# Kernel tuning notes

Hardware: AMD Instinct MI355X
Metric: run time of the kernel (lower is better)

## Reference

```python
import jax, jax.numpy as jnp
import numpy as np

MIN_ROUGHNESS = 0.08
MAX_ROUGHNESS = 0.5
N_MIPS = 6  # 512 -> 16 cubemap mip chain


def _safe_normalize(x, eps=1e-20):
    return x * jax.lax.rsqrt(jnp.clip(jnp.sum(x * x, -1, keepdims=True), eps, None))


def _dot(a, b):
    return jnp.sum(a * b, -1, keepdims=True)


def _cube_face_uv(d):
    # nvdiffrast cube addressing (matches util.cube_to_dir face layout)
    x, y, z = d[..., 0], d[..., 1], d[..., 2]
    ax, ay, az = jnp.abs(x), jnp.abs(y), jnp.abs(z)
    is_x = (ax >= ay) & (ax >= az)
    is_y = (~is_x) & (ay >= az)
    face = jnp.where(is_x, jnp.where(x >= 0, 0, 1),
           jnp.where(is_y, jnp.where(y >= 0, 2, 3), jnp.where(z >= 0, 4, 5)))
    ma = jnp.maximum(jnp.where(is_x, ax, jnp.where(is_y, ay, az)), 1e-20)
    u = jnp.where(face == 0, -z, jnp.where(face == 1, z, jnp.where(face == 5, -x, x))) / ma
    v = jnp.where(face == 2, z, jnp.where(face == 3, -z, -y)) / ma
    return face, u, v


def _bilinear_cube(tex, face, u, v):
    # tex: [6,R,R,C]; face/u/v: [...]; edge-clamped bilinear within the face
    R = tex.shape[1]
    tu = (u * 0.5 + 0.5) * R - 0.5
    tv = (v * 0.5 + 0.5) * R - 0.5
    x0 = jnp.floor(tu); y0 = jnp.floor(tv)
    fx = (tu - x0)[..., None]; fy = (tv - y0)[..., None]
    x0i = jnp.clip(x0, 0, R - 1).astype(jnp.int32)
    x1i = jnp.clip(x0 + 1, 0, R - 1).astype(jnp.int32)
    y0i = jnp.clip(y0, 0, R - 1).astype(jnp.int32)
    y1i = jnp.clip(y0 + 1, 0, R - 1).astype(jnp.int32)
    c00 = tex[face, y0i, x0i]; c01 = tex[face, y0i, x1i]
    c10 = tex[face, y1i, x0i]; c11 = tex[face, y1i, x1i]
    return (c00 * (1 - fx) + c01 * fx) * (1 - fy) + (c10 * (1 - fx) + c11 * fx) * fy


def _sample_cubemap(tex, dirs):
    f, u, v = _cube_face_uv(dirs)
    return _bilinear_cube(tex, f, u, v)


def _sample_2d_clamp(tex, uv):
    # tex: [H,W,C]; uv in [0,1]^2, clamp boundary bilinear (FG LUT lookup)
    H, W = tex.shape[0], tex.shape[1]
    tu = uv[..., 0] * W - 0.5
    tv = uv[..., 1] * H - 0.5
    x0 = jnp.floor(tu); y0 = jnp.floor(tv)
    fx = (tu - x0)[..., None]; fy = (tv - y0)[..., None]
    x0i = jnp.clip(x0, 0, W - 1).astype(jnp.int32)
    x1i = jnp.clip(x0 + 1, 0, W - 1).astype(jnp.int32)
    y0i = jnp.clip(y0, 0, H - 1).astype(jnp.int32)
    y1i = jnp.clip(y0 + 1, 0, H - 1).astype(jnp.int32)
    c00 = tex[y0i, x0i]; c01 = tex[y0i, x1i]
    c10 = tex[y1i, x0i]; c11 = tex[y1i, x1i]
    return (c00 * (1 - fx) + c01 * fx) * (1 - fy) + (c10 * (1 - fx) + c11 * fx) * fy


def _get_mip(r, n_levels):
    lo = (jnp.clip(r, MIN_ROUGHNESS, MAX_ROUGHNESS) - MIN_ROUGHNESS) / (MAX_ROUGHNESS - MIN_ROUGHNESS) * (n_levels - 2)
    hi = (jnp.clip(r, MAX_ROUGHNESS, 1.0) - MAX_ROUGHNESS) / (1.0 - MAX_ROUGHNESS) + (n_levels - 2)
    return jnp.where(r < MAX_ROUGHNESS, lo, hi)


def _linear2srgb(x):
    xs = jnp.where(x > 0.0031308, x, 1.0)  # avoid pow(0) grad issues
    return jnp.where(x > 0.0031308, 1.055 * jnp.power(xs, 1.0 / 2.4) - 0.055, 12.92 * x)


def _avg_pool_cube(c):
    F, R, _, C = c.shape
    return c.reshape(F, R // 2, 2, R // 2, 2, C).mean(axis=(2, 4))


def setup_inputs() -> dict:
    key = jax.random.key(0)
    ks = jax.random.split(key, 10)
    B, H, W = 1, 1024, 1024
    gb_pos = jax.random.normal(ks[0], (B, H, W, 3), jnp.float32)
    gb_normal = _safe_normalize(jax.random.normal(ks[1], (B, H, W, 3), jnp.float32))
    basecolor = jax.random.uniform(ks[2], (B, H, W, 3), jnp.float32)
    metallic = jax.random.uniform(ks[3], (B, H, W, 1), jnp.float32)
    roughness = jax.random.uniform(ks[4], (B, H, W, 1), jnp.float32)
    view_pos = jax.random.normal(ks[5], (1, 1, 1, 3), jnp.float32) * 3.0
    diffuse = jax.random.uniform(ks[6], (6, 16, 16, 3), jnp.float32)
    fg_lut = jax.random.uniform(ks[7], (256, 256, 2), jnp.float32)
    specs = {}
    s = jax.random.uniform(ks[8], (6, 512, 512, 3), jnp.float32)
    for l in range(N_MIPS):
        specs['spec%d' % l] = s
        if l < N_MIPS - 1:
            s = _avg_pool_cube(s)
    return dict(gb_pos=gb_pos, gb_normal=gb_normal, basecolor=basecolor,
                metallic=metallic, roughness=roughness, view_pos=view_pos,
                diffuse=diffuse, fg_lut=fg_lut, **specs)


def reference(gb_pos, gb_normal, basecolor, metallic, roughness, view_pos,
              diffuse, fg_lut, spec0, spec1, spec2, spec3, spec4, spec5):
    specs = [spec0, spec1, spec2, spec3, spec4, spec5]
    L = len(specs)
    metallic = metallic[..., :1]
    wo = _safe_normalize(view_pos - gb_pos)
    diffuse_albedo = (1.0 - metallic) * basecolor
    specular_albedo = 0.04 * (1.0 - metallic) + metallic * basecolor
    reflvec = _safe_normalize(2.0 * _dot(wo, gb_normal) * gb_normal - wo)
    # diffuse IBL: cubemap gather along normal
    ambient = _sample_cubemap(diffuse, gb_normal)
    diffuse_linear = ambient * diffuse_albedo
    # FG LUT gather
    NdotV = jnp.clip(_dot(wo, gb_normal), 1e-4, None)
    fg = _sample_2d_clamp(fg_lut, jnp.concatenate([NdotV, roughness], -1))
    # trilinear (linear-mipmap-linear) specular cubemap gather
    mip = jnp.clip(_get_mip(roughness[..., 0], L), 0.0, L - 1.0)
    face, u, v = _cube_face_uv(reflvec)
    spec = jnp.zeros(gb_pos.shape[:-1] + (spec0.shape[-1],), gb_pos.dtype)
    for l in range(L):
        w = jnp.clip(1.0 - jnp.abs(mip - l), 0.0, 1.0)[..., None]
        spec = spec + w * _bilinear_cube(specs[l], face, u, v)
    reflectance = specular_albedo * fg[..., 0:1] + fg[..., 1:2]
    rgb = spec * reflectance + diffuse_linear
    return _linear2srgb(jnp.clip(rgb, 0.0, 1.0))
```

## Files before the change

kernel.cpp:

```cpp
#include <hip/hip_runtime.h>

struct V3 { float x, y, z; };

__device__ __forceinline__ V3 v3add(V3 a, V3 b){ return {a.x+b.x, a.y+b.y, a.z+b.z}; }
__device__ __forceinline__ V3 v3sub(V3 a, V3 b){ return {a.x-b.x, a.y-b.y, a.z-b.z}; }
__device__ __forceinline__ V3 v3scale(V3 a, float s){ return {a.x*s, a.y*s, a.z*s}; }
__device__ __forceinline__ V3 v3mul(V3 a, V3 b){ return {a.x*b.x, a.y*b.y, a.z*b.z}; }
__device__ __forceinline__ float dot3(V3 a, V3 b){ return fmaf(a.x,b.x, fmaf(a.y,b.y, a.z*b.z)); }
__device__ __forceinline__ V3 nrm3(V3 a){
    float s = rsqrtf(fmaxf(dot3(a,a), 1e-20f));
    return v3scale(a, s);
}

#define OFF0 0
#define OFF1 1572864
#define OFF2 1966080
#define OFF3 2064384
#define OFF4 2088960
#define OFF5 2095104
#define DIFF_OFF 2096640
#define TOTAL_TEXELS 2098176
#define WS_BYTES_NEEDED (TOTAL_TEXELS * 16)

__device__ __forceinline__ void cube_face_uv(V3 d, int& face, float& u, float& v){
    float ax = fabsf(d.x), ay = fabsf(d.y), az = fabsf(d.z);
    bool is_x = (ax >= ay) && (ax >= az);
    bool is_y = (!is_x) && (ay >= az);
    face = is_x ? (d.x >= 0.f ? 0 : 1)
                : (is_y ? (d.y >= 0.f ? 2 : 3)
                        : (d.z >= 0.f ? 4 : 5));
    float ma = fmaxf(is_x ? ax : (is_y ? ay : az), 1e-20f);
    float un = (face == 0) ? -d.z : (face == 1) ? d.z : (face == 5) ? -d.x : d.x;
    float vn = (face == 2) ?  d.z : (face == 3) ? -d.z : -d.y;
    float inv = 1.0f / ma;
    u = un * inv;
    v = vn * inv;
}

struct BilinCoord { int x0i, x1i, y0i, y1i; float fx, fy; };

__device__ __forceinline__ BilinCoord bilin_coord(float u, float v, int R){
    float Rf = (float)R;
    float tu = fmaf(fmaf(u, 0.5f, 0.5f), Rf, -0.5f);
    float tv = fmaf(fmaf(v, 0.5f, 0.5f), Rf, -0.5f);
    float x0 = floorf(tu), y0 = floorf(tv);
    BilinCoord c;
    c.fx = tu - x0; c.fy = tv - y0;
    c.x0i = min(max((int)x0,     0), R-1);
    c.x1i = min(max((int)x0 + 1, 0), R-1);
    c.y0i = min(max((int)y0,     0), R-1);
    c.y1i = min(max((int)y0 + 1, 0), R-1);
    return c;
}

__device__ __forceinline__ V3 bilinear_cube4(const float4* __restrict__ tex, int R,
                                             int face, float u, float v){
    BilinCoord c = bilin_coord(u, v, R);
    const float4* base = tex + (size_t)face * R * R;
    const float4* r0 = base + (size_t)c.y0i * R;
    const float4* r1 = base + (size_t)c.y1i * R;
    float4 a = r0[c.x0i];
    float4 b = r0[c.x1i];
    float4 d = r1[c.x0i];
    float4 e = r1[c.x1i];
    float w00 = (1.f-c.fx)*(1.f-c.fy), w01 = c.fx*(1.f-c.fy);
    float w10 = (1.f-c.fx)*c.fy,       w11 = c.fx*c.fy;
    V3 out;
    out.x = a.x*w00 + b.x*w01 + d.x*w10 + e.x*w11;
    out.y = a.y*w00 + b.y*w01 + d.y*w10 + e.y*w11;
    out.z = a.z*w00 + b.z*w01 + d.z*w10 + e.z*w11;
    return out;
}

__device__ __forceinline__ V3 bilinear_cube3(const float* __restrict__ tex, int R,
                                             int face, float u, float v){
    BilinCoord c = bilin_coord(u, v, R);
    const float* base = tex + (size_t)face * R * R * 3;
    const float* r0 = base + (size_t)c.y0i * R * 3;
    const float* r1 = base + (size_t)c.y1i * R * 3;
    const float* p00 = r0 + 3*c.x0i;
    const float* p01 = r0 + 3*c.x1i;
    const float* p10 = r1 + 3*c.x0i;
    const float* p11 = r1 + 3*c.x1i;
    float a0 = p00[0], a1 = p00[1], a2 = p00[2];
    float b0 = p01[0], b1 = p01[1], b2 = p01[2];
    float d0 = p10[0], d1 = p10[1], d2 = p10[2];
    float e0 = p11[0], e1 = p11[1], e2 = p11[2];
    float w00 = (1.f-c.fx)*(1.f-c.fy), w01 = c.fx*(1.f-c.fy);
    float w10 = (1.f-c.fx)*c.fy,       w11 = c.fx*c.fy;
    V3 out;
    out.x = a0*w00 + b0*w01 + d0*w10 + e0*w11;
    out.y = a1*w00 + b1*w01 + d1*w10 + e1*w11;
    out.z = a2*w00 + b2*w01 + d2*w10 + e2*w11;
    return out;
}

__device__ __forceinline__ void sample_fg(const float* __restrict__ lut,
                                          float u, float v, float& fa, float& fb){
    const int W = 256, H = 256;
    float tu = fmaf(u, (float)W, -0.5f);
    float tv = fmaf(v, (float)H, -0.5f);
    float x0 = floorf(tu), y0 = floorf(tv);
    float fx = tu - x0,    fy = tv - y0;
    int x0i = min(max((int)x0,     0), W-1);
    int x1i = min(max((int)x0 + 1, 0), W-1);
    int y0i = min(max((int)y0,     0), H-1);
    int y1i = min(max((int)y0 + 1, 0), H-1);
    const float2* l2 = (const float2*)lut;
    float2 a = l2[(size_t)y0i*W + x0i];
    float2 b = l2[(size_t)y0i*W + x1i];
    float2 d = l2[(size_t)y1i*W + x0i];
    float2 e = l2[(size_t)y1i*W + x1i];
    float w00 = (1.f-fx)*(1.f-fy), w01 = fx*(1.f-fy);
    float w10 = (1.f-fx)*fy,       w11 = fx*fy;
    fa = a.x*w00 + b.x*w01 + d.x*w10 + e.x*w11;
    fb = a.y*w00 + b.y*w01 + d.y*w10 + e.y*w11;
}

__device__ __forceinline__ float lin2srgb(float x){
    float xs = (x > 0.0031308f) ? x : 1.0f;
    float p  = __builtin_amdgcn_exp2f(__builtin_amdgcn_logf(xs) * (1.0f/2.4f));
    return (x > 0.0031308f) ? fmaf(1.055f, p, -0.055f) : 12.92f * x;
}

__device__ __forceinline__ float clamp01(float x){ return fminf(fmaxf(x, 0.f), 1.f); }

__global__ __launch_bounds__(256)
void pack_kernel(const float* __restrict__ s0, const float* __restrict__ s1,
                 const float* __restrict__ s2, const float* __restrict__ s3,
                 const float* __restrict__ s4, const float* __restrict__ s5,
                 const float* __restrict__ diffuse,
                 float4* __restrict__ ws)
{
    int t = blockIdx.x * blockDim.x + threadIdx.x;
    if (t >= TOTAL_TEXELS) return;
    const float* src; int local;
    if      (t >= DIFF_OFF) { src = diffuse; local = t - DIFF_OFF; }
    else if (t >= OFF5)     { src = s5;      local = t - OFF5; }
    else if (t >= OFF4)     { src = s4;      local = t - OFF4; }
    else if (t >= OFF3)     { src = s3;      local = t - OFF3; }
    else if (t >= OFF2)     { src = s2;      local = t - OFF2; }
    else if (t >= OFF1)     { src = s1;      local = t - OFF1; }
    else                    { src = s0;      local = t; }
    float a = src[3*local], b = src[3*local+1], c = src[3*local+2];
    ws[t] = make_float4(a, b, c, 0.f);
}

template <bool PACKED>
__device__ __forceinline__ void shade_pixel(
    int i,
    const float* __restrict__ gb_pos, const float* __restrict__ gb_normal,
    const float* __restrict__ basecolor, const float* __restrict__ metallic,
    const float* __restrict__ roughness, const float* __restrict__ view_pos,
    const float* __restrict__ diffuse, const float* __restrict__ fg_lut,
    const float* __restrict__ s0, const float* __restrict__ s1,
    const float* __restrict__ s2, const float* __restrict__ s3,
    const float* __restrict__ s4, const float* __restrict__ s5,
    const float4* __restrict__ ws,
    float* __restrict__ out)
{
    V3 pos = { gb_pos[3*i],    gb_pos[3*i+1],    gb_pos[3*i+2] };
    V3 nrm = { gb_normal[3*i], gb_normal[3*i+1], gb_normal[3*i+2] };
    V3 bc  = { basecolor[3*i], basecolor[3*i+1], basecolor[3*i+2] };
    float m = metallic[i];
    float r = roughness[i];
    V3 vp  = { view_pos[0], view_pos[1], view_pos[2] };

    V3 wo = nrm3(v3sub(vp, pos));
    float ndv_raw = dot3(wo, nrm);
    V3 refl = nrm3(v3sub(v3scale(nrm, 2.0f*ndv_raw), wo));

    float one_m = 1.0f - m;
    V3 diff_alb = v3scale(bc, one_m);
    V3 spec_alb = { fmaf(m, bc.x, 0.04f*one_m),
                    fmaf(m, bc.y, 0.04f*one_m),
                    fmaf(m, bc.z, 0.04f*one_m) };

    const float MIN_R = 0.08f, MAX_R = 0.5f;
    float lo = (fminf(fmaxf(r, MIN_R), MAX_R) - MIN_R) / (MAX_R - MIN_R) * 4.0f;
    float hi = (fminf(fmaxf(r, MAX_R), 1.0f) - MAX_R) / (1.0f - MAX_R) + 4.0f;
    float mip = (r < MAX_R) ? lo : hi;
    mip = fminf(fmaxf(mip, 0.0f), 5.0f);
    int l0 = min((int)mip, 5);
    float f = mip - (float)l0;
    int l1 = min(l0 + 1, 5);

    int dface; float du, dv;
    cube_face_uv(nrm, dface, du, dv);
    int sface; float su, sv;
    cube_face_uv(refl, sface, su, sv);
    float NdotV = fmaxf(ndv_raw, 0.0001f);

    V3 ambient, specA, specB;
    if (PACKED) {
        int offA = OFF0;
        offA = (l0 == 1) ? OFF1 : offA; offA = (l0 == 2) ? OFF2 : offA;
        offA = (l0 == 3) ? OFF3 : offA; offA = (l0 == 4) ? OFF4 : offA;
        offA = (l0 == 5) ? OFF5 : offA;
        int offB = OFF0;
        offB = (l1 == 1) ? OFF1 : offB; offB = (l1 == 2) ? OFF2 : offB;
        offB = (l1 == 3) ? OFF3 : offB; offB = (l1 == 4) ? OFF4 : offB;
        offB = (l1 == 5) ? OFF5 : offB;
        ambient = bilinear_cube4(ws + DIFF_OFF, 16, dface, du, dv);
        specA   = bilinear_cube4(ws + offA, 512 >> l0, sface, su, sv);
        specB   = bilinear_cube4(ws + offB, 512 >> l1, sface, su, sv);
    } else {
        const float* tA = s0;
        tA = (l0 == 1) ? s1 : tA; tA = (l0 == 2) ? s2 : tA;
        tA = (l0 == 3) ? s3 : tA; tA = (l0 == 4) ? s4 : tA; tA = (l0 == 5) ? s5 : tA;
        const float* tB = s0;
        tB = (l1 == 1) ? s1 : tB; tB = (l1 == 2) ? s2 : tB;
        tB = (l1 == 3) ? s3 : tB; tB = (l1 == 4) ? s4 : tB; tB = (l1 == 5) ? s5 : tB;
        ambient = bilinear_cube3(diffuse, 16, dface, du, dv);
        specA   = bilinear_cube3(tA, 512 >> l0, sface, su, sv);
        specB   = bilinear_cube3(tB, 512 >> l1, sface, su, sv);
    }

    float fa, fb;
    sample_fg(fg_lut, NdotV, r, fa, fb);

    V3 spec = { specA.x + (specB.x - specA.x) * f,
                specA.y + (specB.y - specA.y) * f,
                specA.z + (specB.z - specA.z) * f };
    V3 reflc = { fmaf(spec_alb.x, fa, fb),
                 fmaf(spec_alb.y, fa, fb),
                 fmaf(spec_alb.z, fa, fb) };
    V3 rgb = v3add(v3mul(spec, reflc), v3mul(ambient, diff_alb));

    out[3*i+0] = lin2srgb(clamp01(rgb.x));
    out[3*i+1] = lin2srgb(clamp01(rgb.y));
    out[3*i+2] = lin2srgb(clamp01(rgb.z));
}

template <bool PACKED>
__global__ __launch_bounds__(256)
void envlight_kernel(const float* __restrict__ gb_pos,
                     const float* __restrict__ gb_normal,
                     const float* __restrict__ basecolor,
                     const float* __restrict__ metallic,
                     const float* __restrict__ roughness,
                     const float* __restrict__ view_pos,
                     const float* __restrict__ diffuse,
                     const float* __restrict__ fg_lut,
                     const float* __restrict__ s0,
                     const float* __restrict__ s1,
                     const float* __restrict__ s2,
                     const float* __restrict__ s3,
                     const float* __restrict__ s4,
                     const float* __restrict__ s5,
                     const float4* __restrict__ ws,
                     float* __restrict__ out,
                     int n)
{
    int i = blockIdx.x * blockDim.x + threadIdx.x;
    if (i >= n) return;
    shade_pixel<PACKED>(i, gb_pos, gb_normal, basecolor, metallic, roughness,
                        view_pos, diffuse, fg_lut, s0, s1, s2, s3, s4, s5, ws, out);
}

extern "C" void kernel_launch(void* const* d_in, const int* in_sizes, int n_in,
                              void* d_out, int out_size, void* d_ws, size_t ws_size,
                              hipStream_t stream) {
    const float* gb_pos    = (const float*)d_in[0];
    const float* gb_normal = (const float*)d_in[1];
    const float* basecolor = (const float*)d_in[2];
    const float* metallic  = (const float*)d_in[3];
    const float* roughness = (const float*)d_in[4];
    const float* view_pos  = (const float*)d_in[5];
    const float* diffuse   = (const float*)d_in[6];
    const float* fg_lut    = (const float*)d_in[7];
    const float* s0        = (const float*)d_in[8];
    const float* s1        = (const float*)d_in[9];
    const float* s2        = (const float*)d_in[10];
    const float* s3        = (const float*)d_in[11];
    const float* s4        = (const float*)d_in[12];
    const float* s5        = (const float*)d_in[13];
    float* out = (float*)d_out;

    int n = in_sizes[0] / 3;
    int block = 256;
    int grid = (n + block - 1) / block;

    if (ws_size >= (size_t)WS_BYTES_NEEDED) {
        float4* ws = (float4*)d_ws;
        int pgrid = (TOTAL_TEXELS + block - 1) / block;
        pack_kernel<<<pgrid, block, 0, stream>>>(s0, s1, s2, s3, s4, s5, diffuse, ws);
        envlight_kernel<true><<<grid, block, 0, stream>>>(gb_pos, gb_normal, basecolor,
            metallic, roughness, view_pos, diffuse, fg_lut,
            s0, s1, s2, s3, s4, s5, ws, out, n);
    } else {
        envlight_kernel<false><<<grid, block, 0, stream>>>(gb_pos, gb_normal, basecolor,
            metallic, roughness, view_pos, diffuse, fg_lut,
            s0, s1, s2, s3, s4, s5, (const float4*)nullptr, out, n);
    }
}
```

Before: 184.2 us.

## Pack horizontal texel pairs as fp16 blocks to halve gathers per bilinear tap

The pack kernel now stores each texel together with its right neighbour as six fp16 values in a 16-byte block, instead of one fp32 RGB texel padded to a float4. Each bilinear lookup then needs two 16-byte loads, one per row, rather than four. The left edge is handled by zeroing fx when x0 is negative, and the right edge by duplicating the last texel in each row. This cuts the number of scattered gather transactions, but texture values lose precision to fp16 and the pack kernel does double reads.

```diff
diff --git a/kernel.cpp b/kernel.cpp
--- a/kernel.cpp
+++ b/kernel.cpp
@@ -1,4 +1,5 @@
 #include <hip/hip_runtime.h>
+#include <hip/hip_fp16.h>
 
 struct V3 { float x, y, z; };
 
@@ -12,6 +13,8 @@
     return v3scale(a, s);
 }
 
+struct __align__(16) PairBlock { __half2 h01, h23, h45, h67; };
+
 #define OFF0 0
 #define OFF1 1572864
 #define OFF2 1966080
@@ -19,8 +22,8 @@
 #define OFF4 2088960
 #define OFF5 2095104
 #define DIFF_OFF 2096640
-#define TOTAL_TEXELS 2098176
-#define WS_BYTES_NEEDED (TOTAL_TEXELS * 16)
+#define TOTAL_BLOCKS 2098176
+#define WS_BYTES_NEEDED (TOTAL_BLOCKS * 16)
 
 __device__ __forceinline__ void cube_face_uv(V3 d, int& face, float& u, float& v){
     float ax = fabsf(d.x), ay = fabsf(d.y), az = fabsf(d.z);
@@ -37,57 +40,54 @@
     v = vn * inv;
 }
 
-struct BilinCoord { int x0i, x1i, y0i, y1i; float fx, fy; };
-
-__device__ __forceinline__ BilinCoord bilin_coord(float u, float v, int R){
+__device__ __forceinline__ void pair_extract(const PairBlock& pb, V3& lo, V3& hi){
+    lo.x = __low2float(pb.h01);  lo.y = __high2float(pb.h01); lo.z = __low2float(pb.h23);
+    hi.x = __high2float(pb.h23); hi.y = __low2float(pb.h45);  hi.z = __high2float(pb.h45);
+}
+
+__device__ __forceinline__ V3 bilinear_pairtex(const PairBlock* __restrict__ lvl, int R,
+                                               int face, float u, float v){
+    float Rf = (float)R;
+    float tu = fmaf(fmaf(u, 0.5f, 0.5f), Rf, -0.5f);
+    float tv = fmaf(fmaf(v, 0.5f, 0.5f), Rf, -0.5f);
+    float x0f = floorf(tu), y0f = floorf(tv);
+    float fx = tu - x0f,    fy = tv - y0f;
+    int x0 = (int)x0f;
+    fx = (x0 < 0) ? 0.f : fx;
+    int xb  = min(max(x0, 0), R-1);
+    int y0i = min(max((int)y0f,     0), R-1);
+    int y1i = min(max((int)y0f + 1, 0), R-1);
+    const PairBlock* fb = lvl + (size_t)face * R * R;
+    PairBlock b0 = fb[(size_t)y0i * R + xb];
+    PairBlock b1 = fb[(size_t)y1i * R + xb];
+    V3 l0, h0, l1, h1;
+    pair_extract(b0, l0, h0);
+    pair_extract(b1, l1, h1);
+    V3 r0 = { l0.x + (h0.x-l0.x)*fx, l0.y + (h0.y-l0.y)*fx, l0.z + (h0.z-l0.z)*fx };
+    V3 r1 = { l1.x + (h1.x-l1.x)*fx, l1.y + (h1.y-l1.y)*fx, l1.z + (h1.z-l1.z)*fx };
+    return { r0.x + (r1.x-r0.x)*fy, r0.y + (r1.y-r0.y)*fy, r0.z + (r1.z-r0.z)*fy };
+}
+
+__device__ __forceinline__ V3 bilinear_cube3(const float* __restrict__ tex, int R,
+                                             int face, float u, float v){
     float Rf = (float)R;
     float tu = fmaf(fmaf(u, 0.5f, 0.5f), Rf, -0.5f);
     float tv = fmaf(fmaf(v, 0.5f, 0.5f), Rf, -0.5f);
     float x0 = floorf(tu), y0 = floorf(tv);
-    BilinCoord c;
-    c.fx = tu - x0; c.fy = tv - y0;
-    c.x0i = min(max((int)x0,     0), R-1);
-    c.x1i = min(max((int)x0 + 1, 0), R-1);
-    c.y0i = min(max((int)y0,     0), R-1);
-    c.y1i = min(max((int)y0 + 1, 0), R-1);
-    return c;
-}
-
-__device__ __forceinline__ V3 bilinear_cube4(const float4* __restrict__ tex, int R,
-                                             int face, float u, float v){
-    BilinCoord c = bilin_coord(u, v, R);
-    const float4* base = tex + (size_t)face * R * R;
-    const float4* r0 = base + (size_t)c.y0i * R;
-    const float4* r1 = base + (size_t)c.y1i * R;
-    float4 a = r0[c.x0i];
-    float4 b = r0[c.x1i];
-    float4 d = r1[c.x0i];
-    float4 e = r1[c.x1i];
-    float w00 = (1.f-c.fx)*(1.f-c.fy), w01 = c.fx*(1.f-c.fy);
-    float w10 = (1.f-c.fx)*c.fy,       w11 = c.fx*c.fy;
-    V3 out;
-    out.x = a.x*w00 + b.x*w01 + d.x*w10 + e.x*w11;
-    out.y = a.y*w00 + b.y*w01 + d.y*w10 + e.y*w11;
-    out.z = a.z*w00 + b.z*w01 + d.z*w10 + e.z*w11;
-    return out;
-}
-
-__device__ __forceinline__ V3 bilinear_cube3(const float* __restrict__ tex, int R,
-                                             int face, float u, float v){
-    BilinCoord c = bilin_coord(u, v, R);
+    float fx = tu - x0,    fy = tv - y0;
+    int x0i = min(max((int)x0,     0), R-1);
+    int x1i = min(max((int)x0 + 1, 0), R-1);
+    int y0i = min(max((int)y0,     0), R-1);
+    int y1i = min(max((int)y0 + 1, 0), R-1);
     const float* base = tex + (size_t)face * R * R * 3;
-    const float* r0 = base + (size_t)c.y0i * R * 3;
-    const float* r1 = base + (size_t)c.y1i * R * 3;
-    const float* p00 = r0 + 3*c.x0i;
-    const float* p01 = r0 + 3*c.x1i;
-    const float* p10 = r1 + 3*c.x0i;
-    const float* p11 = r1 + 3*c.x1i;
-    float a0 = p00[0], a1 = p00[1], a2 = p00[2];
-    float b0 = p01[0], b1 = p01[1], b2 = p01[2];
-    float d0 = p10[0], d1 = p10[1], d2 = p10[2];
-    float e0 = p11[0], e1 = p11[1], e2 = p11[2];
-    float w00 = (1.f-c.fx)*(1.f-c.fy), w01 = c.fx*(1.f-c.fy);
-    float w10 = (1.f-c.fx)*c.fy,       w11 = c.fx*c.fy;
+    const float* r0 = base + (size_t)y0i * R * 3;
+    const float* r1 = base + (size_t)y1i * R * 3;
+    float a0 = r0[3*x0i], a1 = r0[3*x0i+1], a2 = r0[3*x0i+2];
+    float b0 = r0[3*x1i], b1 = r0[3*x1i+1], b2 = r0[3*x1i+2];
+    float d0 = r1[3*x0i], d1 = r1[3*x0i+1], d2 = r1[3*x0i+2];
+    float e0 = r1[3*x1i], e1 = r1[3*x1i+1], e2 = r1[3*x1i+2];
+    float w00 = (1.f-fx)*(1.f-fy), w01 = fx*(1.f-fy);
+    float w10 = (1.f-fx)*fy,       w11 = fx*fy;
     V3 out;
     out.x = a0*w00 + b0*w01 + d0*w10 + e0*w11;
     out.y = a1*w00 + b1*w01 + d1*w10 + e1*w11;
@@ -130,20 +130,27 @@
                  const float* __restrict__ s2, const float* __restrict__ s3,
                  const float* __restrict__ s4, const float* __restrict__ s5,
                  const float* __restrict__ diffuse,
-                 float4* __restrict__ ws)
+                 PairBlock* __restrict__ ws)
 {
     int t = blockIdx.x * blockDim.x + threadIdx.x;
-    if (t >= TOTAL_TEXELS) return;
-    const float* src; int local;
-    if      (t >= DIFF_OFF) { src = diffuse; local = t - DIFF_OFF; }
-    else if (t >= OFF5)     { src = s5;      local = t - OFF5; }
-    else if (t >= OFF4)     { src = s4;      local = t - OFF4; }
-    else if (t >= OFF3)     { src = s3;      local = t - OFF3; }
-    else if (t >= OFF2)     { src = s2;      local = t - OFF2; }
-    else if (t >= OFF1)     { src = s1;      local = t - OFF1; }
-    else                    { src = s0;      local = t; }
-    float a = src[3*local], b = src[3*local+1], c = src[3*local+2];
-    ws[t] = make_float4(a, b, c, 0.f);
+    if (t >= TOTAL_BLOCKS) return;
+    const float* src; int local; int Rmask;
+    if      (t >= DIFF_OFF) { src = diffuse; local = t - DIFF_OFF; Rmask = 15;  }
+    else if (t >= OFF5)     { src = s5;      local = t - OFF5;     Rmask = 15;  }
+    else if (t >= OFF4)     { src = s4;      local = t - OFF4;     Rmask = 31;  }
+    else if (t >= OFF3)     { src = s3;      local = t - OFF3;     Rmask = 63;  }
+    else if (t >= OFF2)     { src = s2;      local = t - OFF2;     Rmask = 127; }
+    else if (t >= OFF1)     { src = s1;      local = t - OFF1;     Rmask = 255; }
+    else                    { src = s0;      local = t;            Rmask = 511; }
+    int nb = ((local & Rmask) == Rmask) ? local : local + 1;
+    float ar = src[3*local], ag = src[3*local+1], ab = src[3*local+2];
+    float br = src[3*nb],    bg = src[3*nb+1],    bb = src[3*nb+2];
+    PairBlock pb;
+    pb.h01 = __floats2half2_rn(ar, ag);
+    pb.h23 = __floats2half2_rn(ab, br);
+    pb.h45 = __floats2half2_rn(bg, bb);
+    pb.h67 = __floats2half2_rn(0.f, 0.f);
+    ws[t] = pb;
 }
 
 template <bool PACKED>
@@ -156,7 +163,7 @@
     const float* __restrict__ s0, const float* __restrict__ s1,
     const float* __restrict__ s2, const float* __restrict__ s3,
     const float* __restrict__ s4, const float* __restrict__ s5,
-    const float4* __restrict__ ws,
+    const PairBlock* __restrict__ ws,
     float* __restrict__ out)
 {
     V3 pos = { gb_pos[3*i],    gb_pos[3*i+1],    gb_pos[3*i+2] };
@@ -201,9 +208,9 @@
         offB = (l1 == 1) ? OFF1 : offB; offB = (l1 == 2) ? OFF2 : offB;
         offB = (l1 == 3) ? OFF3 : offB; offB = (l1 == 4) ? OFF4 : offB;
         offB = (l1 == 5) ? OFF5 : offB;
-        ambient = bilinear_cube4(ws + DIFF_OFF, 16, dface, du, dv);
-        specA   = bilinear_cube4(ws + offA, 512 >> l0, sface, su, sv);
-        specB   = bilinear_cube4(ws + offB, 512 >> l1, sface, su, sv);
+        ambient = bilinear_pairtex(ws + DIFF_OFF, 16, dface, du, dv);
+        specA   = bilinear_pairtex(ws + offA, 512 >> l0, sface, su, sv);
+        specB   = bilinear_pairtex(ws + offB, 512 >> l1, sface, su, sv);
     } else {
         const float* tA = s0;
         tA = (l0 == 1) ? s1 : tA; tA = (l0 == 2) ? s2 : tA;
@@ -248,7 +255,7 @@
                      const float* __restrict__ s3,
                      const float* __restrict__ s4,
                      const float* __restrict__ s5,
-                     const float4* __restrict__ ws,
+                     const PairBlock* __restrict__ ws,
                      float* __restrict__ out,
                      int n)
 {
@@ -282,8 +289,8 @@
     int grid = (n + block - 1) / block;
 
     if (ws_size >= (size_t)WS_BYTES_NEEDED) {
-        float4* ws = (float4*)d_ws;
-        int pgrid = (TOTAL_TEXELS + block - 1) / block;
+        PairBlock* ws = (PairBlock*)d_ws;
+        int pgrid = (TOTAL_BLOCKS + block - 1) / block;
         pack_kernel<<<pgrid, block, 0, stream>>>(s0, s1, s2, s3, s4, s5, diffuse, ws);
         envlight_kernel<true><<<grid, block, 0, stream>>>(gb_pos, gb_normal, basecolor,
             metallic, roughness, view_pos, diffuse, fg_lut,
@@ -291,6 +298,6 @@
     } else {
         envlight_kernel<false><<<grid, block, 0, stream>>>(gb_pos, gb_normal, basecolor,
             metallic, roughness, view_pos, diffuse, fg_lut,
-            s0, s1, s2, s3, s4, s5, (const float4*)nullptr, out, n);
+            s0, s1, s2, s3, s4, s5, (const PairBlock*)nullptr, out, n);
     }
 }
```

Result: faster. 172.9 us (-6.1%).
